# Optimization experiments

Measured on AMD Instinct MI355X. Metric: run time of the kernel, lower is better.

## Reference

```python
import jax, jax.numpy as jnp
import numpy as np

H2 = 128  # 2*hidden_dim

def setup_inputs() -> dict:
    key = jax.random.key(0)
    k1, k2, k3 = jax.random.split(key, 3)
    B, Lb, Lp = 64, 1024, 1024
    body = jax.random.normal(k1, (B, Lb, H2), dtype=jnp.float32)
    pun = jax.random.normal(k2, (B, Lp, H2), dtype=jnp.float32)
    w_u = jax.random.normal(k3, (3 * H2, 1), dtype=jnp.float32)
    return {"batch_size": B, "body": body, "pun": pun, "w_u": w_u}

def reference(batch_size, body, pun, w_u):
    # score[b,i,j] = [body_i ; pun_j ; body_i*pun_j] @ w_u
    # Decompose w_u into the three 128-dim blocks so the double loop fuses
    # into two matvecs plus one weighted batched GEMM.
    w = w_u[:, 0]
    w1, w2, w3 = w[:H2], w[H2:2 * H2], w[2 * H2:]
    s_body = jnp.einsum('bid,d->bi', body, w1)          # [B, Lb]
    s_pun = jnp.einsum('bjd,d->bj', pun, w2)            # [B, Lp]
    s_cross = jnp.einsum('bid,bjd->bij', body * w3, pun)  # [B, Lb, Lp]
    return s_cross + s_body[:, :, None] + s_pun[:, None, :]
```

## Files before the change

### kernel.cpp

```cpp
#include <hip/hip_runtime.h>


#define LSEQ 1024
#define H2K  128

typedef __attribute__((ext_vector_type(8))) short bfrag;
typedef __attribute__((ext_vector_type(4))) float f32x4;

__device__ __forceinline__ short f2bf(float x) {
    unsigned u = __float_as_uint(x);
    unsigned r = (u + 0x7fff + ((u >> 16) & 1)) >> 16;
    return (short)r;
}

__global__ __launch_bounds__(512, 4) void align_fused(
    const float* __restrict__ body, const float* __restrict__ pun,
    const float* __restrict__ w_u, float* __restrict__ out)
{
    __shared__ __align__(16) short Cb[4096];
    __shared__ __align__(16) short Pb[8192];
    __shared__ __align__(16) float sb[128];
    __shared__ __align__(16) float sp[256];

    const int nwg = gridDim.x;
    const int bid = blockIdx.x;
    const int tid = (bid & 7) * (nwg >> 3) + (bid >> 3);
    const int bb = tid >> 5;
    const int r5 = tid & 31;
    const int ti = (r5 >> 2) * 128;
    const int tj = (r5 & 3) * 256;

    const int t    = threadIdx.x;
    const int lane = t & 63;
    const int w    = t >> 6;

    const int srow = w * 16 + (lane & 15);
    const int k8   = lane >> 4;

    const float4* bp  = (const float4*)(body + (size_t)(bb * LSEQ + ti + srow) * H2K) + k8 * 2;
    const float4* p1  = (const float4*)(pun  + (size_t)(bb * LSEQ + tj + srow) * H2K) + k8 * 2;
    const float4* p2  = (const float4*)(pun  + (size_t)(bb * LSEQ + tj + 128 + srow) * H2K) + k8 * 2;
    const float4* w1v = (const float4*)(w_u          ) + k8 * 2;
    const float4* w2v = (const float4*)(w_u +     H2K) + k8 * 2;
    const float4* w3v = (const float4*)(w_u + 2 * H2K) + k8 * 2;

    const int jg = w & 3;
    const int ig = w >> 2;
    f32x4 acc[4][4] = {};
    float db = 0.f, dp1 = 0.f, dp2 = 0.f;

    for (int kt = 0; kt < 4; ++kt) {
        if (kt) __syncthreads();

        const float4 xb0 = bp[kt * 8],  xb1 = bp[kt * 8 + 1];
        const float4 u30 = w3v[kt * 8], u31 = w3v[kt * 8 + 1];
        const float4 u10 = w1v[kt * 8], u11 = w1v[kt * 8 + 1];
        db += xb0.x * u10.x + xb0.y * u10.y + xb0.z * u10.z + xb0.w * u10.w
            + xb1.x * u11.x + xb1.y * u11.y + xb1.z * u11.z + xb1.w * u11.w;
        bfrag fb;
        fb[0] = f2bf(xb0.x * u30.x); fb[1] = f2bf(xb0.y * u30.y);
        fb[2] = f2bf(xb0.z * u30.z); fb[3] = f2bf(xb0.w * u30.w);
        fb[4] = f2bf(xb1.x * u31.x); fb[5] = f2bf(xb1.y * u31.y);
        fb[6] = f2bf(xb1.z * u31.z); fb[7] = f2bf(xb1.w * u31.w);
        *(bfrag*)&Cb[t * 8] = fb;

        const float4 y10 = p1[kt * 8],  y11 = p1[kt * 8 + 1];
        const float4 y20 = p2[kt * 8],  y21 = p2[kt * 8 + 1];
        const float4 u20 = w2v[kt * 8], u21 = w2v[kt * 8 + 1];
        dp1 += y10.x * u20.x + y10.y * u20.y + y10.z * u20.z + y10.w * u20.w
             + y11.x * u21.x + y11.y * u21.y + y11.z * u21.z + y11.w * u21.w;
        dp2 += y20.x * u20.x + y20.y * u20.y + y20.z * u20.z + y20.w * u20.w
             + y21.x * u21.x + y21.y * u21.y + y21.z * u21.z + y21.w * u21.w;
        bfrag f1, f2;
        f1[0] = f2bf(y10.x); f1[1] = f2bf(y10.y); f1[2] = f2bf(y10.z); f1[3] = f2bf(y10.w);
        f1[4] = f2bf(y11.x); f1[5] = f2bf(y11.y); f1[6] = f2bf(y11.z); f1[7] = f2bf(y11.w);
        f2[0] = f2bf(y20.x); f2[1] = f2bf(y20.y); f2[2] = f2bf(y20.z); f2[3] = f2bf(y20.w);
        f2[4] = f2bf(y21.x); f2[5] = f2bf(y21.y); f2[6] = f2bf(y21.z); f2[7] = f2bf(y21.w);
        *(bfrag*)&Pb[t * 8]         = f1;
        *(bfrag*)&Pb[(512 + t) * 8] = f2;

        __syncthreads();

        bfrag ph[4];
#pragma unroll
        for (int jj = 0; jj < 4; ++jj)
            ph[jj] = *(const bfrag*)&Pb[((jg * 4 + jj) * 64 + lane) * 8];
#pragma unroll
        for (int ii = 0; ii < 4; ++ii) {
            const bfrag ch = *(const bfrag*)&Cb[((ig * 4 + ii) * 64 + lane) * 8];
#pragma unroll
            for (int jj = 0; jj < 4; ++jj)
                acc[jj][ii] = __builtin_amdgcn_mfma_f32_16x16x32_bf16(ph[jj], ch, acc[jj][ii], 0, 0, 0);
        }
    }

    db  += __shfl_xor(db, 16);  db  += __shfl_xor(db, 32);
    dp1 += __shfl_xor(dp1, 16); dp1 += __shfl_xor(dp1, 32);
    dp2 += __shfl_xor(dp2, 16); dp2 += __shfl_xor(dp2, 32);
    if (k8 == 0) {
        sb[srow] = db;
        sp[srow] = dp1;
        sp[128 + srow] = dp2;
    }
    __syncthreads();

    const int qd = lane >> 4, ln = lane & 15;
#pragma unroll
    for (int jj = 0; jj < 4; ++jj) {
        const int jl = (jg * 4 + jj) * 16 + qd * 4;
        const float4 spv = *(const float4*)&sp[jl];
#pragma unroll
        for (int ii = 0; ii < 4; ++ii) {
            const int rl = (ig * 4 + ii) * 16 + ln;
            const float sbv = sb[rl];
            const f32x4 a = acc[jj][ii];
            float4 r = { a[0] + sbv + spv.x, a[1] + sbv + spv.y,
                         a[2] + sbv + spv.z, a[3] + sbv + spv.w };
            *(float4*)&out[(size_t)(bb * LSEQ + ti + rl) * LSEQ + tj + jl] = r;
        }
    }
}

extern "C" void kernel_launch(void* const* d_in, const int* in_sizes, int n_in,
                              void* d_out, int out_size, void* d_ws, size_t ws_size,
                              hipStream_t stream) {
    const float* body = (const float*)d_in[1];
    const float* pun  = (const float*)d_in[2];
    const float* w_u  = (const float*)d_in[3];
    float* out = (float*)d_out;
    const int B = in_sizes[1] / (LSEQ * H2K);

    dim3 g(B * 32, 1, 1);
    align_fused<<<g, 512, 0, stream>>>(body, pun, w_u, out);
}
```

Measured before the change: 376.6 us.

## Shrink output tile to 128x128, stage full K in LDS, nontemporal stores

Result: slower. 394.3 us (+4.7%).

```diff
diff --git a/kernel.cpp b/kernel.cpp
--- a/kernel.cpp
+++ b/kernel.cpp
@@ -17,18 +17,18 @@
     const float* __restrict__ body, const float* __restrict__ pun,
     const float* __restrict__ w_u, float* __restrict__ out)
 {
-    __shared__ __align__(16) short Cb[4096];
-    __shared__ __align__(16) short Pb[8192];
-    __shared__ __align__(16) float sb[128];
-    __shared__ __align__(16) float sp[256];
+    __shared__ __align__(16) short Cb[16384];
+    __shared__ __align__(16) short Pb[16384];
+    __shared__ float sb[128];
+    __shared__ float sp[128];
 
     const int nwg = gridDim.x;
     const int bid = blockIdx.x;
     const int tid = (bid & 7) * (nwg >> 3) + (bid >> 3);
-    const int bb = tid >> 5;
-    const int r5 = tid & 31;
-    const int ti = (r5 >> 2) * 128;
-    const int tj = (r5 & 3) * 256;
+    const int bb = tid >> 6;
+    const int r6 = tid & 63;
+    const int ti = (r6 >> 3) * 128;
+    const int tj = (r6 & 7) * 128;
 
     const int t    = threadIdx.x;
     const int lane = t & 63;
@@ -38,85 +38,81 @@
     const int k8   = lane >> 4;
 
     const float4* bp  = (const float4*)(body + (size_t)(bb * LSEQ + ti + srow) * H2K) + k8 * 2;
-    const float4* p1  = (const float4*)(pun  + (size_t)(bb * LSEQ + tj + srow) * H2K) + k8 * 2;
-    const float4* p2  = (const float4*)(pun  + (size_t)(bb * LSEQ + tj + 128 + srow) * H2K) + k8 * 2;
+    const float4* pp  = (const float4*)(pun  + (size_t)(bb * LSEQ + tj + srow) * H2K) + k8 * 2;
     const float4* w1v = (const float4*)(w_u          ) + k8 * 2;
     const float4* w2v = (const float4*)(w_u +     H2K) + k8 * 2;
     const float4* w3v = (const float4*)(w_u + 2 * H2K) + k8 * 2;
 
-    const int jg = w & 3;
-    const int ig = w >> 2;
-    f32x4 acc[4][4] = {};
-    float db = 0.f, dp1 = 0.f, dp2 = 0.f;
+    float db = 0.f, dp = 0.f;
+#pragma unroll
+    for (int kc = 0; kc < 4; ++kc) {
+        const float4 xb0 = bp[kc * 8],  xb1 = bp[kc * 8 + 1];
+        const float4 yp0 = pp[kc * 8],  yp1 = pp[kc * 8 + 1];
+        const float4 u10 = w1v[kc * 8], u11 = w1v[kc * 8 + 1];
+        const float4 u20 = w2v[kc * 8], u21 = w2v[kc * 8 + 1];
+        const float4 u30 = w3v[kc * 8], u31 = w3v[kc * 8 + 1];
 
-    for (int kt = 0; kt < 4; ++kt) {
-        if (kt) __syncthreads();
-
-        const float4 xb0 = bp[kt * 8],  xb1 = bp[kt * 8 + 1];
-        const float4 u30 = w3v[kt * 8], u31 = w3v[kt * 8 + 1];
-        const float4 u10 = w1v[kt * 8], u11 = w1v[kt * 8 + 1];
         db += xb0.x * u10.x + xb0.y * u10.y + xb0.z * u10.z + xb0.w * u10.w
             + xb1.x * u11.x + xb1.y * u11.y + xb1.z * u11.z + xb1.w * u11.w;
-        bfrag fb;
+        dp += yp0.x * u20.x + yp0.y * u20.y + yp0.z * u20.z + yp0.w * u20.w
+            + yp1.x * u21.x + yp1.y * u21.y + yp1.z * u21.z + yp1.w * u21.w;
+
+        bfrag fb, fp;
         fb[0] = f2bf(xb0.x * u30.x); fb[1] = f2bf(xb0.y * u30.y);
         fb[2] = f2bf(xb0.z * u30.z); fb[3] = f2bf(xb0.w * u30.w);
         fb[4] = f2bf(xb1.x * u31.x); fb[5] = f2bf(xb1.y * u31.y);
         fb[6] = f2bf(xb1.z * u31.z); fb[7] = f2bf(xb1.w * u31.w);
-        *(bfrag*)&Cb[t * 8] = fb;
-
-        const float4 y10 = p1[kt * 8],  y11 = p1[kt * 8 + 1];
-        const float4 y20 = p2[kt * 8],  y21 = p2[kt * 8 + 1];
-        const float4 u20 = w2v[kt * 8], u21 = w2v[kt * 8 + 1];
-        dp1 += y10.x * u20.x + y10.y * u20.y + y10.z * u20.z + y10.w * u20.w
-             + y11.x * u21.x + y11.y * u21.y + y11.z * u21.z + y11.w * u21.w;
-        dp2 += y20.x * u20.x + y20.y * u20.y + y20.z * u20.z + y20.w * u20.w
-             + y21.x * u21.x + y21.y * u21.y + y21.z * u21.z + y21.w * u21.w;
-        bfrag f1, f2;
-        f1[0] = f2bf(y10.x); f1[1] = f2bf(y10.y); f1[2] = f2bf(y10.z); f1[3] = f2bf(y10.w);
-        f1[4] = f2bf(y11.x); f1[5] = f2bf(y11.y); f1[6] = f2bf(y11.z); f1[7] = f2bf(y11.w);
-        f2[0] = f2bf(y20.x); f2[1] = f2bf(y20.y); f2[2] = f2bf(y20.z); f2[3] = f2bf(y20.w);
-        f2[4] = f2bf(y21.x); f2[5] = f2bf(y21.y); f2[6] = f2bf(y21.z); f2[7] = f2bf(y21.w);
-        *(bfrag*)&Pb[t * 8]         = f1;
-        *(bfrag*)&Pb[(512 + t) * 8] = f2;
-
-        __syncthreads();
-
-        bfrag ph[4];
-#pragma unroll
-        for (int jj = 0; jj < 4; ++jj)
-            ph[jj] = *(const bfrag*)&Pb[((jg * 4 + jj) * 64 + lane) * 8];
-#pragma unroll
-        for (int ii = 0; ii < 4; ++ii) {
-            const bfrag ch = *(const bfrag*)&Cb[((ig * 4 + ii) * 64 + lane) * 8];
-#pragma unroll
-            for (int jj = 0; jj < 4; ++jj)
-                acc[jj][ii] = __builtin_amdgcn_mfma_f32_16x16x32_bf16(ph[jj], ch, acc[jj][ii], 0, 0, 0);
-        }
+        fp[0] = f2bf(yp0.x); fp[1] = f2bf(yp0.y);
+        fp[2] = f2bf(yp0.z); fp[3] = f2bf(yp0.w);
+        fp[4] = f2bf(yp1.x); fp[5] = f2bf(yp1.y);
+        fp[6] = f2bf(yp1.z); fp[7] = f2bf(yp1.w);
+        *(bfrag*)&Cb[(kc * 512 + t) * 8] = fb;
+        *(bfrag*)&Pb[(kc * 512 + t) * 8] = fp;
     }
 
-    db  += __shfl_xor(db, 16);  db  += __shfl_xor(db, 32);
-    dp1 += __shfl_xor(dp1, 16); dp1 += __shfl_xor(dp1, 32);
-    dp2 += __shfl_xor(dp2, 16); dp2 += __shfl_xor(dp2, 32);
+    db += __shfl_xor(db, 16); db += __shfl_xor(db, 32);
+    dp += __shfl_xor(dp, 16); dp += __shfl_xor(dp, 32);
     if (k8 == 0) {
         sb[srow] = db;
-        sp[srow] = dp1;
-        sp[128 + srow] = dp2;
+        sp[srow] = dp;
     }
+
     __syncthreads();
+
+    const int wrow = w >> 2;
+    const int wcol = w & 3;
+    f32x4 acc[2][4] = {};
+#pragma unroll
+    for (int kc = 0; kc < 4; ++kc) {
+        bfrag ph[2], cb[4];
+#pragma unroll
+        for (int jj = 0; jj < 2; ++jj)
+            ph[jj] = *(const bfrag*)&Pb[((kc * 8 + wcol * 2 + jj) * 64 + lane) * 8];
+#pragma unroll
+        for (int ii = 0; ii < 4; ++ii)
+            cb[ii] = *(const bfrag*)&Cb[((kc * 8 + wrow * 4 + ii) * 64 + lane) * 8];
+#pragma unroll
+        for (int jj = 0; jj < 2; ++jj)
+#pragma unroll
+            for (int ii = 0; ii < 4; ++ii)
+                acc[jj][ii] = __builtin_amdgcn_mfma_f32_16x16x32_bf16(
+                    ph[jj], cb[ii], acc[jj][ii], 0, 0, 0);
+    }
 
     const int qd = lane >> 4, ln = lane & 15;
 #pragma unroll
-    for (int jj = 0; jj < 4; ++jj) {
-        const int jl = (jg * 4 + jj) * 16 + qd * 4;
-        const float4 spv = *(const float4*)&sp[jl];
+    for (int jj = 0; jj < 2; ++jj) {
+        const int jl = (wcol * 2 + jj) * 16 + qd * 4;
+        const f32x4 spv = *(const f32x4*)&sp[jl];
 #pragma unroll
         for (int ii = 0; ii < 4; ++ii) {
-            const int rl = (ig * 4 + ii) * 16 + ln;
+            const int rl = (wrow * 4 + ii) * 16 + ln;
             const float sbv = sb[rl];
             const f32x4 a = acc[jj][ii];
-            float4 r = { a[0] + sbv + spv.x, a[1] + sbv + spv.y,
-                         a[2] + sbv + spv.z, a[3] + sbv + spv.w };
-            *(float4*)&out[(size_t)(bb * LSEQ + ti + rl) * LSEQ + tj + jl] = r;
+            f32x4 r = { a[0] + sbv + spv[0], a[1] + sbv + spv[1],
+                        a[2] + sbv + spv[2], a[3] + sbv + spv[3] };
+            __builtin_nontemporal_store(
+                r, (f32x4*)&out[(size_t)(bb * LSEQ + ti + rl) * LSEQ + tj + jl]);
         }
     }
 }
@@ -130,6 +126,6 @@
     float* out = (float*)d_out;
     const int B = in_sizes[1] / (LSEQ * H2K);
 
-    dim3 g(B * 32, 1, 1);
+    dim3 g(B * 64, 1, 1);
     align_fused<<<g, 512, 0, stream>>>(body, pun, w_u, out);
 }
```
